# Kernel tuning notes

Hardware: AMD Instinct MI355X
Metric: run time of the kernel (lower is better)

The kernel has to match this reference:

```python
import jax, jax.numpy as jnp
import numpy as np

E = 8          # number of routed experts
TOP_K = 2      # experts per token
D = 2048       # hidden size
DFF = 1408     # per-expert intermediate
DFF_S = 2816   # shared-expert intermediate (2 shared experts fused)
B, S = 2, 2048


def setup_inputs() -> dict:
    key = jax.random.key(0)
    ks = jax.random.split(key, 8)
    sc = 0.02
    return {
        "hidden_states": jax.random.normal(ks[0], (B, S, D), jnp.float32),
        "gate_weight": jax.random.normal(ks[1], (E, D), jnp.float32) * sc,
        "w_gate": jax.random.normal(ks[2], (E, DFF, D), jnp.float32) * sc,
        "w_up": jax.random.normal(ks[3], (E, DFF, D), jnp.float32) * sc,
        "w_down": jax.random.normal(ks[4], (E, D, DFF), jnp.float32) * sc,
        "w_shared_gate": jax.random.normal(ks[5], (DFF_S, D), jnp.float32) * sc,
        "w_shared_up": jax.random.normal(ks[6], (DFF_S, D), jnp.float32) * sc,
        "w_shared_down": jax.random.normal(ks[7], (D, DFF_S), jnp.float32) * sc,
    }


def reference(hidden_states, gate_weight, w_gate, w_up, w_down,
              w_shared_gate, w_shared_up, w_shared_down):
    orig_shape = hidden_states.shape
    x = hidden_states.reshape(-1, orig_shape[-1])      # [T, D]

    # --- router (computed under no_grad in the original) ---
    logits = x @ gate_weight.T                          # [T, E]
    scores = jax.nn.softmax(logits, axis=-1)
    topk_w, topk_idx = jax.lax.top_k(scores, TOP_K)     # [T, K]
    topk_w = topk_w / jnp.sum(topk_w, axis=-1, keepdims=True)
    topk_w = jax.lax.stop_gradient(topk_w)
    topk_idx = jax.lax.stop_gradient(topk_idx)

    # dense combine weights [T, E] (equivalent to the masked per-expert loop +
    # weighted sum over the top-k copies)
    combine = jnp.einsum('tk,tke->te', topk_w,
                         jax.nn.one_hot(topk_idx, E, dtype=x.dtype))

    # --- routed experts: SwiGLU MLP per expert, dense over E ---
    g = jnp.einsum('td,efd->etf', x, w_gate)            # [E, T, DFF]
    u = jnp.einsum('td,efd->etf', x, w_up)
    h = jax.nn.silu(g) * u
    expert_out = jnp.einsum('etf,edf->etd', h, w_down)  # [E, T, D]
    y = jnp.einsum('etd,te->td', expert_out, combine)   # [T, D]

    # --- shared experts on the identity ---
    sh = jax.nn.silu(x @ w_shared_gate.T) * (x @ w_shared_up.T)
    y = y + sh @ w_shared_down.T

    return y.reshape(orig_shape)
```

## Files before the change

kernel.cpp:

```cpp
#include <hip/hip_runtime.h>
#include <stdint.h>
#include <stdio.h>

#define T_TOK 4096
#define DMODEL 2048
#define NEXP 8
#define DFF 1408
#define DFFS 2816
#define NSLOT 8192

#define GU_GRID (16 * 22 + 39 * 11)
#define DN_GRID (16 * 8 + 39 * 8)

typedef unsigned short u16;
typedef short s16x8 __attribute__((ext_vector_type(8)));
typedef unsigned short u16x4 __attribute__((ext_vector_type(4)));
typedef __bf16 bf16x8 __attribute__((ext_vector_type(8)));
typedef float f32x4 __attribute__((ext_vector_type(4)));

__device__ __forceinline__ u16 f2bf(float f) {
  uint32_t u = __builtin_bit_cast(uint32_t, f);
  u += 0x7fffu + ((u >> 16) & 1u);
  return (u16)(u >> 16);
}
__device__ __forceinline__ float bf2f(u16 h) {
  uint32_t u = ((uint32_t)h) << 16;
  return __builtin_bit_cast(float, u);
}

__device__ __forceinline__ void gl16(const u16* g, u16* l) {
  __builtin_amdgcn_global_load_lds((const __attribute__((address_space(1))) void*)g,
                                   (__attribute__((address_space(3))) void*)l,
                                   16, 0, 0);
}

#define BARRIER() asm volatile("s_barrier" ::: "memory")

__global__ void k_convert(const float* __restrict__ in, u16* __restrict__ out, int n8) {
  int i = blockIdx.x * 256 + threadIdx.x;
  if (i >= n8) return;
  float4 a = ((const float4*)in)[2 * i];
  float4 b = ((const float4*)in)[2 * i + 1];
  s16x8 r;
  r[0] = (short)f2bf(a.x); r[1] = (short)f2bf(a.y);
  r[2] = (short)f2bf(a.z); r[3] = (short)f2bf(a.w);
  r[4] = (short)f2bf(b.x); r[5] = (short)f2bf(b.y);
  r[6] = (short)f2bf(b.z); r[7] = (short)f2bf(b.w);
  ((s16x8*)out)[i] = r;
}

__global__ void k_zero(int* __restrict__ counts) {
  if (threadIdx.x < NEXP) counts[threadIdx.x] = 0;
}

__global__ void k_router(const float* __restrict__ x, const float* __restrict__ gw,
                         u16* __restrict__ xb,
                         float* __restrict__ tkw, int* __restrict__ tki,
                         int* __restrict__ counts) {
  __shared__ double sm[NEXP];
  int t = blockIdx.x;
  int tid = threadIdx.x;
  int lane = tid & 63, wv = tid >> 6;
  const float4* xr = (const float4*)(x + (size_t)t * DMODEL);
  const float4* gr = (const float4*)gw;
  int e0 = wv * 2, e1 = e0 + 1;
  double a0 = 0.0, a1 = 0.0;
#pragma unroll
  for (int it = 0; it < DMODEL / 4 / 64; ++it) {
    int idx = it * 64 + lane;
    float4 xv = xr[idx];
    float4 g0 = gr[e0 * (DMODEL / 4) + idx];
    float4 g1 = gr[e1 * (DMODEL / 4) + idx];
    a0 += (double)xv.x * g0.x + (double)xv.y * g0.y +
          (double)xv.z * g0.z + (double)xv.w * g0.w;
    a1 += (double)xv.x * g1.x + (double)xv.y * g1.y +
          (double)xv.z * g1.z + (double)xv.w * g1.w;
    if (wv == 0) {
      u16x4 r = { f2bf(xv.x), f2bf(xv.y), f2bf(xv.z), f2bf(xv.w) };
      ((u16x4*)(xb + (size_t)t * DMODEL))[idx] = r;
    }
  }
#pragma unroll
  for (int off = 32; off; off >>= 1) {
    a0 += __shfl_down(a0, off, 64);
    a1 += __shfl_down(a1, off, 64);
  }
  if (lane == 0) { sm[e0] = a0; sm[e1] = a1; }
  __syncthreads();
  if (tid == 0) {
    double acc[NEXP];
#pragma unroll
    for (int e = 0; e < NEXP; ++e) acc[e] = sm[e];
    int i0 = 0; double v0 = acc[0];
    for (int e = 1; e < NEXP; ++e) if (acc[e] > v0) { v0 = acc[e]; i0 = e; }
    int i1 = -1; double v1 = -1e300;
    for (int e = 0; e < NEXP; ++e) if (e != i0 && acc[e] > v1) { v1 = acc[e]; i1 = e; }
    double r = exp(v1 - v0);
    float w0 = (float)(1.0 / (1.0 + r));
    float w1 = 1.0f - w0;
    tkw[2 * t] = w0; tkw[2 * t + 1] = w1;
    tki[2 * t] = i0; tki[2 * t + 1] = i1;
    atomicAdd(&counts[i0], 1);
    atomicAdd(&counts[i1], 1);
  }
}

__global__ void k_scan(const int* __restrict__ counts, int* __restrict__ offs,
                       int* __restrict__ cursor) {
  if (threadIdx.x == 0) {
    int s = 0;
    for (int e = 0; e < NEXP; ++e) { offs[e] = s; cursor[e] = s; s += counts[e]; }
    offs[NEXP] = s;
  }
}

__global__ void k_assign(const int* __restrict__ tki, int* __restrict__ cursor,
                         int* __restrict__ pos, int* __restrict__ slot_tok) {
  int t = blockIdx.x * 256 + threadIdx.x;
  if (t >= T_TOK) return;
#pragma unroll
  for (int k = 0; k < 2; ++k) {
    int e = tki[2 * t + k];
    int p = atomicAdd(&cursor[e], 1);
    pos[2 * t + k] = p;
    slot_tok[p] = t;
  }
}

__global__ void k_sched(const int* __restrict__ counts, int* __restrict__ tblGU,
                        int* __restrict__ tblDN, int* __restrict__ nact) {
  if (threadIdx.x != 0 || blockIdx.x != 0) return;
  int g = 0, d = 0;
  for (int m = 0; m < T_TOK / 256; ++m) {
    for (int nb = 0; nb < DFFS * 2 / 256; ++nb)
      tblGU[g++] = (int)(0x80000000u | (m << 12) | nb);
    for (int nb = 0; nb < DMODEL / 256; ++nb)
      tblDN[d++] = (int)(0x80000000u | (m << 12) | nb);
  }
  for (int e = 0; e < NEXP; ++e) {
    int mb = (counts[e] + 255) >> 8;
    for (int m = 0; m < mb; ++m) {
      for (int nb = 0; nb < DFF * 2 / 256; ++nb)
        tblGU[g++] = (e << 24) | (m << 12) | nb;
      for (int nb = 0; nb < DMODEL / 256; ++nb)
        tblDN[d++] = (e << 24) | (m << 12) | nb;
    }
  }
  nact[0] = g; nact[1] = d;
}

template <int PHASE>
__launch_bounds__(512, 2)
__global__ void k_gemm8(const int* __restrict__ tbl, const int* __restrict__ nact,
                        const u16* __restrict__ xb,
                        const u16* __restrict__ hr, const u16* __restrict__ hs,
                        const u16* __restrict__ wbg, const u16* __restrict__ wbu,
                        const u16* __restrict__ wbd,
                        const u16* __restrict__ wbsg, const u16* __restrict__ wbsu,
                        const u16* __restrict__ wbsd,
                        u16* __restrict__ P1r, u16* __restrict__ P2r,
                        u16* __restrict__ P1s, u16* __restrict__ P2s,
                        u16* __restrict__ yr, float* __restrict__ out,
                        const int* __restrict__ offs, const int* __restrict__ counts,
                        const int* __restrict__ slot_tok) {
  __shared__ __attribute__((aligned(16))) u16 lds[2 * 32768];

  if ((int)blockIdx.x >= nact[PHASE]) return;
  const int desc = tbl[blockIdx.x];
  const bool shrd = desc < 0;
  const int e = (desc >> 24) & 0xF;
  const int m0 = ((desc >> 12) & 0xFFF) * 256;
  const int n0 = (desc & 0xFFF) * 256;

  const u16 *A, *B1, *B2;
  u16 *C1, *C2;
  float* OF = nullptr;
  int base, cnt, nsplit, K;
  bool gather = false;
  if constexpr (PHASE == 0) {
    K = DMODEL;
    if (shrd) {
      A = xb; base = 0; cnt = T_TOK;
      B1 = wbsg; B2 = wbsu; C1 = P1s; C2 = P2s; nsplit = DFFS;
    } else {
      A = xb; gather = true; base = offs[e]; cnt = counts[e];
      size_t es = (size_t)e * DFF * DMODEL;
      B1 = wbg + es; B2 = wbu + es; C1 = P1r; C2 = P2r; nsplit = DFF;
    }
  } else {
    nsplit = DMODEL;
    if (shrd) {
      A = hs; base = 0; cnt = T_TOK; K = DFFS;
      B1 = B2 = wbsd; OF = out; C1 = C2 = nullptr;
    } else {
      A = hr; base = offs[e]; cnt = counts[e]; K = DFF;
      B1 = B2 = wbd + (size_t)e * DMODEL * DFF; C1 = C2 = yr;
    }
  }
  const int NT = K >> 6;

  int tid = threadIdx.x;
  int lane = tid & 63, wv = tid >> 6;
  int wm = wv >> 2, wn = wv & 3;
  int fr = lane & 15, fq = lane >> 4;

  int srow = tid >> 3;
  int sslot = (tid & 7) ^ (srow & 7);
  const u16* ap[4]; const u16* bp[4];
#pragma unroll
  for (int h = 0; h < 4; ++h) {
    int r = h * 64 + srow;
    int ra = m0 + r; ra = ra < cnt ? ra : cnt - 1;
    int ga = gather ? slot_tok[base + ra] : base + ra;
    ap[h] = A + (size_t)ga * K + sslot * 8;
    int nc = n0 + r;
    const u16* bb = (nc >= nsplit) ? (B2 + (size_t)(nc - nsplit) * K)
                                   : (B1 + (size_t)nc * K);
    bp[h] = bb + sslot * 8;
  }

#define STG_A(h, bufi, kt) gl16(ap[h] + (size_t)(kt) * 64, \
                                lds + (bufi) * 32768 + (h) * 4096 + wv * 512)
#define STG_B(h, bufi, kt) gl16(bp[h] + (size_t)(kt) * 64, \
                                lds + (bufi) * 32768 + 16384 + (h) * 4096 + wv * 512)

  int sKs0 = ((0 + fq) ^ (fr & 7)) * 8;
  int sKs1 = ((4 + fq) ^ (fr & 7)) * 8;
  int aBase = wm * 8192 + fr * 64;
  int bBase = 16384 + (wn >> 1) * 8192 + ((wn & 1) * 64 + fr) * 64;

  f32x4 acc[8][4];
#pragma unroll
  for (int i = 0; i < 8; ++i)
#pragma unroll
    for (int j = 0; j < 4; ++j) acc[i][j] = (f32x4){0.f, 0.f, 0.f, 0.f};

  STG_A(0, 0, 0); STG_A(2, 0, 0);
  STG_B(0, 0, 0); STG_B(1, 0, 0);
  STG_B(2, 0, 0); STG_B(3, 0, 0);
  STG_A(1, 0, 0); STG_A(3, 0, 0);
  STG_A(0, 1, 1); STG_A(2, 1, 1);

  bf16x8 af[4][2], bkA[2][2], bkB[2][2];
  for (int t = 0; t < NT; ++t) {
    const int buf = t & 1, nbuf = buf ^ 1;
    const u16* lbuf = lds + buf * 32768;
    const bool hn1 = (t + 1) < NT, hn2 = (t + 2) < NT;

    if (t == NT - 1) asm volatile("s_waitcnt vmcnt(2)" ::: "memory");
    else             asm volatile("s_waitcnt vmcnt(4)" ::: "memory");
    BARRIER();
    __builtin_amdgcn_sched_barrier(0);
#pragma unroll
    for (int il = 0; il < 4; ++il) {
      af[il][0] = *(const bf16x8*)(lbuf + aBase + il * 1024 + sKs0);
      af[il][1] = *(const bf16x8*)(lbuf + aBase + il * 1024 + sKs1);
    }
#pragma unroll
    for (int jl = 0; jl < 2; ++jl) {
      bkA[jl][0] = *(const bf16x8*)(lbuf + bBase + jl * 1024 + sKs0);
      bkA[jl][1] = *(const bf16x8*)(lbuf + bBase + jl * 1024 + sKs1);
    }
    if (hn1) { STG_B(0, nbuf, t + 1); STG_B(1, nbuf, t + 1); }
    asm volatile("s_waitcnt lgkmcnt(0)" ::: "memory");
    __builtin_amdgcn_sched_barrier(0);
    __builtin_amdgcn_s_setprio(1);
#pragma unroll
    for (int il = 0; il < 4; ++il)
#pragma unroll
      for (int jl = 0; jl < 2; ++jl) {
        acc[il][jl] = __builtin_amdgcn_mfma_f32_16x16x32_bf16(af[il][0], bkA[jl][0], acc[il][jl], 0, 0, 0);
        acc[il][jl] = __builtin_amdgcn_mfma_f32_16x16x32_bf16(af[il][1], bkA[jl][1], acc[il][jl], 0, 0, 0);
      }
    __builtin_amdgcn_s_setprio(0);
    __builtin_amdgcn_sched_barrier(0);

    BARRIER();
    __builtin_amdgcn_sched_barrier(0);
#pragma unroll
    for (int jl = 0; jl < 2; ++jl) {
      bkB[jl][0] = *(const bf16x8*)(lbuf + bBase + (2 + jl) * 1024 + sKs0);
      bkB[jl][1] = *(const bf16x8*)(lbuf + bBase + (2 + jl) * 1024 + sKs1);
    }
    if (hn1) { STG_B(2, nbuf, t + 1); STG_B(3, nbuf, t + 1); }
    asm volatile("s_waitcnt lgkmcnt(0)" ::: "memory");
    __builtin_amdgcn_sched_barrier(0);
    __builtin_amdgcn_s_setprio(1);
#pragma unroll
    for (int il = 0; il < 4; ++il)
#pragma unroll
      for (int jl = 0; jl < 2; ++jl) {
        acc[il][2 + jl] = __builtin_amdgcn_mfma_f32_16x16x32_bf16(af[il][0], bkB[jl][0], acc[il][2 + jl], 0, 0, 0);
        acc[il][2 + jl] = __builtin_amdgcn_mfma_f32_16x16x32_bf16(af[il][1], bkB[jl][1], acc[il][2 + jl], 0, 0, 0);
      }
    __builtin_amdgcn_s_setprio(0);
    __builtin_amdgcn_sched_barrier(0);

    if (t == NT - 1) asm volatile("s_waitcnt vmcnt(0)" ::: "memory");
    else             asm volatile("s_waitcnt vmcnt(6)" ::: "memory");
    BARRIER();
    __builtin_amdgcn_sched_barrier(0);
#pragma unroll
    for (int il = 0; il < 4; ++il) {
      af[il][0] = *(const bf16x8*)(lbuf + aBase + (4 + il) * 1024 + sKs0);
      af[il][1] = *(const bf16x8*)(lbuf + aBase + (4 + il) * 1024 + sKs1);
    }
    if (hn1) { STG_A(1, nbuf, t + 1); STG_A(3, nbuf, t + 1); }
    asm volatile("s_waitcnt lgkmcnt(0)" ::: "memory");
    __builtin_amdgcn_sched_barrier(0);
    __builtin_amdgcn_s_setprio(1);
#pragma unroll
    for (int il = 0; il < 4; ++il)
#pragma unroll
      for (int jl = 0; jl < 2; ++jl) {
        acc[4 + il][jl] = __builtin_amdgcn_mfma_f32_16x16x32_bf16(af[il][0], bkA[jl][0], acc[4 + il][jl], 0, 0, 0);
        acc[4 + il][jl] = __builtin_amdgcn_mfma_f32_16x16x32_bf16(af[il][1], bkA[jl][1], acc[4 + il][jl], 0, 0, 0);
      }
    __builtin_amdgcn_s_setprio(0);
    __builtin_amdgcn_sched_barrier(0);

    BARRIER();
    __builtin_amdgcn_sched_barrier(0);
#pragma unroll
    for (int jl = 0; jl < 2; ++jl) {
      bkB[jl][0] = *(const bf16x8*)(lbuf + bBase + (2 + jl) * 1024 + sKs0);
      bkB[jl][1] = *(const bf16x8*)(lbuf + bBase + (2 + jl) * 1024 + sKs1);
    }
    if (hn2) { STG_A(0, buf, t + 2); STG_A(2, buf, t + 2); }
    asm volatile("s_waitcnt lgkmcnt(0)" ::: "memory");
    __builtin_amdgcn_sched_barrier(0);
    __builtin_amdgcn_s_setprio(1);
#pragma unroll
    for (int il = 0; il < 4; ++il)
#pragma unroll
      for (int jl = 0; jl < 2; ++jl) {
        acc[4 + il][2 + jl] = __builtin_amdgcn_mfma_f32_16x16x32_bf16(af[il][0], bkB[jl][0], acc[4 + il][2 + jl], 0, 0, 0);
        acc[4 + il][2 + jl] = __builtin_amdgcn_mfma_f32_16x16x32_bf16(af[il][1], bkB[jl][1], acc[4 + il][2 + jl], 0, 0, 0);
      }
    __builtin_amdgcn_s_setprio(0);
    __builtin_amdgcn_sched_barrier(0);
  }
#undef STG_A
#undef STG_B

#pragma unroll
  for (int i = 0; i < 8; ++i) {
    int row_t = wm * 128 + i * 16 + fq * 4;
#pragma unroll
    for (int r = 0; r < 4; ++r) {
      int m = m0 + row_t + r;
      if (m >= cnt) continue;
      size_t rowoff = (size_t)(base + m) * (size_t)nsplit;
#pragma unroll
      for (int j = 0; j < 4; ++j) {
        int col_t = n0 + wn * 64 + j * 16 + fr;
        float v = acc[i][j][r];
        if (PHASE == 1 && shrd)      OF[rowoff + col_t] = v;
        else if (col_t >= nsplit)    C2[rowoff + col_t - nsplit] = f2bf(v);
        else                         C1[rowoff + col_t] = f2bf(v);
      }
    }
  }
}

__global__ void k_silu2(const u16* __restrict__ g1, const u16* __restrict__ u1,
                        u16* __restrict__ h1, int n1,
                        const u16* __restrict__ g2, const u16* __restrict__ u2,
                        u16* __restrict__ h2, int n2) {
  int i = blockIdx.x * 256 + threadIdx.x;
  const u16 *g, *u; u16* h; int idx;
  if (i < n1) { g = g1; u = u1; h = h1; idx = i; }
  else { idx = i - n1; if (idx >= n2) return; g = g2; u = u2; h = h2; }
  s16x8 gv = ((const s16x8*)g)[idx];
  s16x8 uv = ((const s16x8*)u)[idx];
  s16x8 hv;
#pragma unroll
  for (int j = 0; j < 8; ++j) {
    float gf = bf2f((u16)gv[j]);
    float uf = bf2f((u16)uv[j]);
    float s = gf / (1.f + __expf(-gf));
    hv[j] = (short)f2bf(s * uf);
  }
  ((s16x8*)h)[idx] = hv;
}

__global__ void k_combine(float* __restrict__ y, const u16* __restrict__ yr,
                          const float* __restrict__ tkw, const int* __restrict__ pos) {
  int t = blockIdx.x;
  int i = threadIdx.x;
  float w0 = tkw[2 * t], w1 = tkw[2 * t + 1];
  size_t p0 = (size_t)pos[2 * t] * DMODEL, p1 = (size_t)pos[2 * t + 1] * DMODEL;
  int d0 = i * 8;
  s16x8 a = *(const s16x8*)(yr + p0 + d0);
  s16x8 b = *(const s16x8*)(yr + p1 + d0);
  float* yo = y + (size_t)t * DMODEL + d0;
#pragma unroll
  for (int j = 0; j < 8; ++j)
    yo[j] += w0 * bf2f((u16)a[j]) + w1 * bf2f((u16)b[j]);
}

extern "C" void kernel_launch(void* const* d_in, const int* in_sizes, int n_in,
                              void* d_out, int out_size, void* d_ws, size_t ws_size,
                              hipStream_t stream) {
  const float* x   = (const float*)d_in[0];
  const float* gw  = (const float*)d_in[1];
  const float* wg  = (const float*)d_in[2];
  const float* wu  = (const float*)d_in[3];
  const float* wd  = (const float*)d_in[4];
  const float* wsg = (const float*)d_in[5];
  const float* wsu = (const float*)d_in[6];
  const float* wsd = (const float*)d_in[7];
  float* out = (float*)d_out;

  char* ws = (char*)d_ws;
  size_t o = 0;
  auto alloc = [&](size_t bytes) -> void* {
    void* p = ws + o;
    o += (bytes + 255) & ~(size_t)255;
    return p;
  };
  u16* xb   = (u16*)alloc((size_t)T_TOK * DMODEL * 2);
  u16* wbg  = (u16*)alloc((size_t)NEXP * DFF * DMODEL * 2);
  u16* wbu  = (u16*)alloc((size_t)NEXP * DFF * DMODEL * 2);
  u16* wbd  = (u16*)alloc((size_t)NEXP * DMODEL * DFF * 2);
  u16* wbsg = (u16*)alloc((size_t)DFFS * DMODEL * 2);
  u16* wbsu = (u16*)alloc((size_t)DFFS * DMODEL * 2);
  u16* wbsd = (u16*)alloc((size_t)DMODEL * DFFS * 2);
  u16* P1r  = (u16*)alloc((size_t)NSLOT * DFF * 2);
  u16* P1s  = (u16*)alloc((size_t)T_TOK * DFFS * 2);
  u16* P2r  = (u16*)alloc((size_t)NSLOT * DFF * 2);
  u16* P2s  = (u16*)alloc((size_t)T_TOK * DFFS * 2);
  u16* yr   = P2r;
  float* tkw = (float*)alloc((size_t)T_TOK * 2 * 4);
  int* tki   = (int*)alloc((size_t)T_TOK * 2 * 4);
  int* pos   = (int*)alloc((size_t)T_TOK * 2 * 4);
  int* slot_tok = (int*)alloc((size_t)NSLOT * 4);
  int* counts   = (int*)alloc(64);
  int* offs     = (int*)alloc(64);
  int* cursor   = (int*)alloc(64);
  int* tblGU    = (int*)alloc(GU_GRID * 4);
  int* tblDN    = (int*)alloc(DN_GRID * 4);
  int* nact     = (int*)alloc(64);
  if (o > ws_size) {
    fprintf(stderr, "kernel_launch: ws too small: need %zu have %zu\n", o, ws_size);
    return;
  }

  {
    int n8w = NEXP * DFF * DMODEL / 8;
    k_convert<<<(n8w + 255) / 256, 256, 0, stream>>>(wg, wbg, n8w);
    k_convert<<<(n8w + 255) / 256, 256, 0, stream>>>(wu, wbu, n8w);
    k_convert<<<(n8w + 255) / 256, 256, 0, stream>>>(wd, wbd, n8w);
    int n8s = DFFS * DMODEL / 8;
    k_convert<<<(n8s + 255) / 256, 256, 0, stream>>>(wsg, wbsg, n8s);
    k_convert<<<(n8s + 255) / 256, 256, 0, stream>>>(wsu, wbsu, n8s);
    k_convert<<<(n8s + 255) / 256, 256, 0, stream>>>(wsd, wbsd, n8s);
  }

  k_zero<<<1, 64, 0, stream>>>(counts);
  k_router<<<T_TOK, 256, 0, stream>>>(x, gw, xb, tkw, tki, counts);
  k_scan<<<1, 64, 0, stream>>>(counts, offs, cursor);
  k_assign<<<(T_TOK + 255) / 256, 256, 0, stream>>>(tki, cursor, pos, slot_tok);
  k_sched<<<1, 64, 0, stream>>>(counts, tblGU, tblDN, nact);

  k_gemm8<0><<<GU_GRID, 512, 0, stream>>>(
      tblGU, nact, xb, nullptr, nullptr,
      wbg, wbu, wbd, wbsg, wbsu, wbsd,
      P1r, P2r, P1s, P2s, yr, out, offs, counts, slot_tok);

  {
    int n1 = NSLOT * DFF / 8, n2 = T_TOK * DFFS / 8;
    k_silu2<<<(n1 + n2 + 255) / 256, 256, 0, stream>>>(
        P1r, P2r, P1r, n1, P1s, P2s, P1s, n2);
  }

  k_gemm8<1><<<DN_GRID, 512, 0, stream>>>(
      tblDN, nact, xb, P1r, P1s,
      wbg, wbu, wbd, wbsg, wbsu, wbsd,
      P1r, P2r, P1s, P2s, yr, out, offs, counts, slot_tok);

  k_combine<<<T_TOK, 256, 0, stream>>>(out, yr, tkw, pos);
}
```

Baseline: 590.4 us.

## Fuse weight conversions, merge scan/sched kernels, and software-pipeline GEMM LDS reads

Merges the six fp32-to-bf16 weight conversion launches into one grid-stride kernel and folds the scan and schedule-table kernels into a single launch. It also restructures the GEMM main loop so the next tile's A/B fragments are read from LDS while the current MFMAs run, cutting the barriers per K-step from four to two. This is meant to reduce launch overhead and LDS-read stalls in the GEMMs. In exchange it needs more fragment registers, which may hurt occupancy, and it changes the vmcnt wait accounting, which must stay correct.

```diff
diff --git a/kernel.cpp b/kernel.cpp
--- a/kernel.cpp
+++ b/kernel.cpp
@@ -36,17 +36,39 @@
 
 #define BARRIER() asm volatile("s_barrier" ::: "memory")
 
-__global__ void k_convert(const float* __restrict__ in, u16* __restrict__ out, int n8) {
-  int i = blockIdx.x * 256 + threadIdx.x;
-  if (i >= n8) return;
-  float4 a = ((const float4*)in)[2 * i];
-  float4 b = ((const float4*)in)[2 * i + 1];
-  s16x8 r;
-  r[0] = (short)f2bf(a.x); r[1] = (short)f2bf(a.y);
-  r[2] = (short)f2bf(a.z); r[3] = (short)f2bf(a.w);
-  r[4] = (short)f2bf(b.x); r[5] = (short)f2bf(b.y);
-  r[6] = (short)f2bf(b.z); r[7] = (short)f2bf(b.w);
-  ((s16x8*)out)[i] = r;
+__global__ void k_convert6(const float* __restrict__ s0, u16* __restrict__ d0, int n0,
+                           const float* __restrict__ s1, u16* __restrict__ d1, int n1,
+                           const float* __restrict__ s2, u16* __restrict__ d2, int n2,
+                           const float* __restrict__ s3, u16* __restrict__ d3, int n3,
+                           const float* __restrict__ s4, u16* __restrict__ d4, int n4,
+                           const float* __restrict__ s5, u16* __restrict__ d5, int n5) {
+  int total = n0 + n1 + n2 + n3 + n4 + n5;
+  int stride = gridDim.x * 256;
+  for (int i = blockIdx.x * 256 + threadIdx.x; i < total; i += stride) {
+    const float* s; u16* d; int k = i;
+    if (k < n0) { s = s0; d = d0; }
+    else { k -= n0;
+      if (k < n1) { s = s1; d = d1; }
+      else { k -= n1;
+        if (k < n2) { s = s2; d = d2; }
+        else { k -= n2;
+          if (k < n3) { s = s3; d = d3; }
+          else { k -= n3;
+            if (k < n4) { s = s4; d = d4; }
+            else { k -= n4; s = s5; d = d5; }
+          }
+        }
+      }
+    }
+    float4 a = ((const float4*)s)[2 * k];
+    float4 b = ((const float4*)s)[2 * k + 1];
+    s16x8 r;
+    r[0] = (short)f2bf(a.x); r[1] = (short)f2bf(a.y);
+    r[2] = (short)f2bf(a.z); r[3] = (short)f2bf(a.w);
+    r[4] = (short)f2bf(b.x); r[5] = (short)f2bf(b.y);
+    r[6] = (short)f2bf(b.z); r[7] = (short)f2bf(b.w);
+    ((s16x8*)d)[k] = r;
+  }
 }
 
 __global__ void k_zero(int* __restrict__ counts) {
@@ -105,31 +127,13 @@
   }
 }
 
-__global__ void k_scan(const int* __restrict__ counts, int* __restrict__ offs,
-                       int* __restrict__ cursor) {
-  if (threadIdx.x == 0) {
-    int s = 0;
-    for (int e = 0; e < NEXP; ++e) { offs[e] = s; cursor[e] = s; s += counts[e]; }
-    offs[NEXP] = s;
-  }
-}
-
-__global__ void k_assign(const int* __restrict__ tki, int* __restrict__ cursor,
-                         int* __restrict__ pos, int* __restrict__ slot_tok) {
-  int t = blockIdx.x * 256 + threadIdx.x;
-  if (t >= T_TOK) return;
-#pragma unroll
-  for (int k = 0; k < 2; ++k) {
-    int e = tki[2 * t + k];
-    int p = atomicAdd(&cursor[e], 1);
-    pos[2 * t + k] = p;
-    slot_tok[p] = t;
-  }
-}
-
-__global__ void k_sched(const int* __restrict__ counts, int* __restrict__ tblGU,
-                        int* __restrict__ tblDN, int* __restrict__ nact) {
+__global__ void k_scan_sched(const int* __restrict__ counts, int* __restrict__ offs,
+                             int* __restrict__ cursor, int* __restrict__ tblGU,
+                             int* __restrict__ tblDN, int* __restrict__ nact) {
   if (threadIdx.x != 0 || blockIdx.x != 0) return;
+  int s = 0;
+  for (int e = 0; e < NEXP; ++e) { offs[e] = s; cursor[e] = s; s += counts[e]; }
+  offs[NEXP] = s;
   int g = 0, d = 0;
   for (int m = 0; m < T_TOK / 256; ++m) {
     for (int nb = 0; nb < DFFS * 2 / 256; ++nb)
@@ -147,6 +151,19 @@
     }
   }
   nact[0] = g; nact[1] = d;
+}
+
+__global__ void k_assign(const int* __restrict__ tki, int* __restrict__ cursor,
+                         int* __restrict__ pos, int* __restrict__ slot_tok) {
+  int t = blockIdx.x * 256 + threadIdx.x;
+  if (t >= T_TOK) return;
+#pragma unroll
+  for (int k = 0; k < 2; ++k) {
+    int e = tki[2 * t + k];
+    int p = atomicAdd(&cursor[e], 1);
+    pos[2 * t + k] = p;
+    slot_tok[p] = t;
+  }
 }
 
 template <int PHASE>
@@ -235,110 +252,104 @@
 #pragma unroll
     for (int j = 0; j < 4; ++j) acc[i][j] = (f32x4){0.f, 0.f, 0.f, 0.f};
 
-  STG_A(0, 0, 0); STG_A(2, 0, 0);
-  STG_B(0, 0, 0); STG_B(1, 0, 0);
-  STG_B(2, 0, 0); STG_B(3, 0, 0);
-  STG_A(1, 0, 0); STG_A(3, 0, 0);
-  STG_A(0, 1, 1); STG_A(2, 1, 1);
-
-  bf16x8 af[4][2], bkA[2][2], bkB[2][2];
+  STG_A(0, 0, 0); STG_A(1, 0, 0); STG_A(2, 0, 0); STG_A(3, 0, 0);
+  STG_B(0, 0, 0); STG_B(1, 0, 0); STG_B(2, 0, 0); STG_B(3, 0, 0);
+  if (NT > 1) { STG_A(0, 1, 1); STG_A(1, 1, 1); STG_A(2, 1, 1); STG_A(3, 1, 1); }
+  if (NT > 1) asm volatile("s_waitcnt vmcnt(4)" ::: "memory");
+  else        asm volatile("s_waitcnt vmcnt(0)" ::: "memory");
+  BARRIER();
+  __builtin_amdgcn_sched_barrier(0);
+
+  bf16x8 rAa[4][2], rAb[4][2], rB01[2][2], rB23[2][2];
+#pragma unroll
+  for (int il = 0; il < 4; ++il) {
+    rAa[il][0] = *(const bf16x8*)(lds + aBase + il * 1024 + sKs0);
+    rAa[il][1] = *(const bf16x8*)(lds + aBase + il * 1024 + sKs1);
+  }
+#pragma unroll
+  for (int jl = 0; jl < 2; ++jl) {
+    rB01[jl][0] = *(const bf16x8*)(lds + bBase + jl * 1024 + sKs0);
+    rB01[jl][1] = *(const bf16x8*)(lds + bBase + jl * 1024 + sKs1);
+  }
+
   for (int t = 0; t < NT; ++t) {
     const int buf = t & 1, nbuf = buf ^ 1;
     const u16* lbuf = lds + buf * 32768;
+    const u16* lbufN = lds + nbuf * 32768;
     const bool hn1 = (t + 1) < NT, hn2 = (t + 2) < NT;
 
-    if (t == NT - 1) asm volatile("s_waitcnt vmcnt(2)" ::: "memory");
-    else             asm volatile("s_waitcnt vmcnt(4)" ::: "memory");
+#pragma unroll
+    for (int jl = 0; jl < 2; ++jl) {
+      rB23[jl][0] = *(const bf16x8*)(lbuf + bBase + (2 + jl) * 1024 + sKs0);
+      rB23[jl][1] = *(const bf16x8*)(lbuf + bBase + (2 + jl) * 1024 + sKs1);
+    }
+    if (hn1) { STG_B(0, nbuf, t + 1); STG_B(1, nbuf, t + 1); }
+    __builtin_amdgcn_s_setprio(1);
+#pragma unroll
+    for (int il = 0; il < 4; ++il)
+#pragma unroll
+      for (int jl = 0; jl < 2; ++jl) {
+        acc[il][jl] = __builtin_amdgcn_mfma_f32_16x16x32_bf16(rAa[il][0], rB01[jl][0], acc[il][jl], 0, 0, 0);
+        acc[il][jl] = __builtin_amdgcn_mfma_f32_16x16x32_bf16(rAa[il][1], rB01[jl][1], acc[il][jl], 0, 0, 0);
+      }
+    __builtin_amdgcn_s_setprio(0);
+
+#pragma unroll
+    for (int il = 0; il < 4; ++il) {
+      rAb[il][0] = *(const bf16x8*)(lbuf + aBase + (4 + il) * 1024 + sKs0);
+      rAb[il][1] = *(const bf16x8*)(lbuf + aBase + (4 + il) * 1024 + sKs1);
+    }
+    if (hn1) { STG_B(2, nbuf, t + 1); STG_B(3, nbuf, t + 1); }
+    __builtin_amdgcn_s_setprio(1);
+#pragma unroll
+    for (int il = 0; il < 4; ++il)
+#pragma unroll
+      for (int jl = 0; jl < 2; ++jl) {
+        acc[il][2 + jl] = __builtin_amdgcn_mfma_f32_16x16x32_bf16(rAa[il][0], rB23[jl][0], acc[il][2 + jl], 0, 0, 0);
+        acc[il][2 + jl] = __builtin_amdgcn_mfma_f32_16x16x32_bf16(rAa[il][1], rB23[jl][1], acc[il][2 + jl], 0, 0, 0);
+      }
+    __builtin_amdgcn_s_setprio(0);
+
+    asm volatile("s_waitcnt lgkmcnt(0)" ::: "memory");
     BARRIER();
     __builtin_amdgcn_sched_barrier(0);
-#pragma unroll
-    for (int il = 0; il < 4; ++il) {
-      af[il][0] = *(const bf16x8*)(lbuf + aBase + il * 1024 + sKs0);
-      af[il][1] = *(const bf16x8*)(lbuf + aBase + il * 1024 + sKs1);
-    }
-#pragma unroll
-    for (int jl = 0; jl < 2; ++jl) {
-      bkA[jl][0] = *(const bf16x8*)(lbuf + bBase + jl * 1024 + sKs0);
-      bkA[jl][1] = *(const bf16x8*)(lbuf + bBase + jl * 1024 + sKs1);
-    }
-    if (hn1) { STG_B(0, nbuf, t + 1); STG_B(1, nbuf, t + 1); }
-    asm volatile("s_waitcnt lgkmcnt(0)" ::: "memory");
-    __builtin_amdgcn_sched_barrier(0);
+    if (hn2) { STG_A(0, buf, t + 2); STG_A(1, buf, t + 2); }
     __builtin_amdgcn_s_setprio(1);
 #pragma unroll
     for (int il = 0; il < 4; ++il)
 #pragma unroll
       for (int jl = 0; jl < 2; ++jl) {
-        acc[il][jl] = __builtin_amdgcn_mfma_f32_16x16x32_bf16(af[il][0], bkA[jl][0], acc[il][jl], 0, 0, 0);
-        acc[il][jl] = __builtin_amdgcn_mfma_f32_16x16x32_bf16(af[il][1], bkA[jl][1], acc[il][jl], 0, 0, 0);
+        acc[4 + il][jl] = __builtin_amdgcn_mfma_f32_16x16x32_bf16(rAb[il][0], rB01[jl][0], acc[4 + il][jl], 0, 0, 0);
+        acc[4 + il][jl] = __builtin_amdgcn_mfma_f32_16x16x32_bf16(rAb[il][1], rB01[jl][1], acc[4 + il][jl], 0, 0, 0);
       }
     __builtin_amdgcn_s_setprio(0);
-    __builtin_amdgcn_sched_barrier(0);
-
-    BARRIER();
-    __builtin_amdgcn_sched_barrier(0);
-#pragma unroll
-    for (int jl = 0; jl < 2; ++jl) {
-      bkB[jl][0] = *(const bf16x8*)(lbuf + bBase + (2 + jl) * 1024 + sKs0);
-      bkB[jl][1] = *(const bf16x8*)(lbuf + bBase + (2 + jl) * 1024 + sKs1);
-    }
-    if (hn1) { STG_B(2, nbuf, t + 1); STG_B(3, nbuf, t + 1); }
-    asm volatile("s_waitcnt lgkmcnt(0)" ::: "memory");
-    __builtin_amdgcn_sched_barrier(0);
+
+    if (hn1) {
+      if (hn2) asm volatile("s_waitcnt vmcnt(2)" ::: "memory");
+      else     asm volatile("s_waitcnt vmcnt(0)" ::: "memory");
+      BARRIER();
+      __builtin_amdgcn_sched_barrier(0);
+      if (hn2) { STG_A(2, buf, t + 2); STG_A(3, buf, t + 2); }
+#pragma unroll
+      for (int il = 0; il < 4; ++il) {
+        rAa[il][0] = *(const bf16x8*)(lbufN + aBase + il * 1024 + sKs0);
+        rAa[il][1] = *(const bf16x8*)(lbufN + aBase + il * 1024 + sKs1);
+      }
+#pragma unroll
+      for (int jl = 0; jl < 2; ++jl) {
+        rB01[jl][0] = *(const bf16x8*)(lbufN + bBase + jl * 1024 + sKs0);
+        rB01[jl][1] = *(const bf16x8*)(lbufN + bBase + jl * 1024 + sKs1);
+      }
+    }
     __builtin_amdgcn_s_setprio(1);
 #pragma unroll
     for (int il = 0; il < 4; ++il)
 #pragma unroll
       for (int jl = 0; jl < 2; ++jl) {
-        acc[il][2 + jl] = __builtin_amdgcn_mfma_f32_16x16x32_bf16(af[il][0], bkB[jl][0], acc[il][2 + jl], 0, 0, 0);
-        acc[il][2 + jl] = __builtin_amdgcn_mfma_f32_16x16x32_bf16(af[il][1], bkB[jl][1], acc[il][2 + jl], 0, 0, 0);
+        acc[4 + il][2 + jl] = __builtin_amdgcn_mfma_f32_16x16x32_bf16(rAb[il][0], rB23[jl][0], acc[4 + il][2 + jl], 0, 0, 0);
+        acc[4 + il][2 + jl] = __builtin_amdgcn_mfma_f32_16x16x32_bf16(rAb[il][1], rB23[jl][1], acc[4 + il][2 + jl], 0, 0, 0);
       }
     __builtin_amdgcn_s_setprio(0);
-    __builtin_amdgcn_sched_barrier(0);
-
-    if (t == NT - 1) asm volatile("s_waitcnt vmcnt(0)" ::: "memory");
-    else             asm volatile("s_waitcnt vmcnt(6)" ::: "memory");
-    BARRIER();
-    __builtin_amdgcn_sched_barrier(0);
-#pragma unroll
-    for (int il = 0; il < 4; ++il) {
-      af[il][0] = *(const bf16x8*)(lbuf + aBase + (4 + il) * 1024 + sKs0);
-      af[il][1] = *(const bf16x8*)(lbuf + aBase + (4 + il) * 1024 + sKs1);
-    }
-    if (hn1) { STG_A(1, nbuf, t + 1); STG_A(3, nbuf, t + 1); }
-    asm volatile("s_waitcnt lgkmcnt(0)" ::: "memory");
-    __builtin_amdgcn_sched_barrier(0);
-    __builtin_amdgcn_s_setprio(1);
-#pragma unroll
-    for (int il = 0; il < 4; ++il)
-#pragma unroll
-      for (int jl = 0; jl < 2; ++jl) {
-        acc[4 + il][jl] = __builtin_amdgcn_mfma_f32_16x16x32_bf16(af[il][0], bkA[jl][0], acc[4 + il][jl], 0, 0, 0);
-        acc[4 + il][jl] = __builtin_amdgcn_mfma_f32_16x16x32_bf16(af[il][1], bkA[jl][1], acc[4 + il][jl], 0, 0, 0);
-      }
-    __builtin_amdgcn_s_setprio(0);
-    __builtin_amdgcn_sched_barrier(0);
-
-    BARRIER();
-    __builtin_amdgcn_sched_barrier(0);
-#pragma unroll
-    for (int jl = 0; jl < 2; ++jl) {
-      bkB[jl][0] = *(const bf16x8*)(lbuf + bBase + (2 + jl) * 1024 + sKs0);
-      bkB[jl][1] = *(const bf16x8*)(lbuf + bBase + (2 + jl) * 1024 + sKs1);
-    }
-    if (hn2) { STG_A(0, buf, t + 2); STG_A(2, buf, t + 2); }
-    asm volatile("s_waitcnt lgkmcnt(0)" ::: "memory");
-    __builtin_amdgcn_sched_barrier(0);
-    __builtin_amdgcn_s_setprio(1);
-#pragma unroll
-    for (int il = 0; il < 4; ++il)
-#pragma unroll
-      for (int jl = 0; jl < 2; ++jl) {
-        acc[4 + il][2 + jl] = __builtin_amdgcn_mfma_f32_16x16x32_bf16(af[il][0], bkB[jl][0], acc[4 + il][2 + jl], 0, 0, 0);
-        acc[4 + il][2 + jl] = __builtin_amdgcn_mfma_f32_16x16x32_bf16(af[il][1], bkB[jl][1], acc[4 + il][2 + jl], 0, 0, 0);
-      }
-    __builtin_amdgcn_s_setprio(0);
-    __builtin_amdgcn_sched_barrier(0);
   }
 #undef STG_A
 #undef STG_B
@@ -448,20 +459,15 @@
 
   {
     int n8w = NEXP * DFF * DMODEL / 8;
-    k_convert<<<(n8w + 255) / 256, 256, 0, stream>>>(wg, wbg, n8w);
-    k_convert<<<(n8w + 255) / 256, 256, 0, stream>>>(wu, wbu, n8w);
-    k_convert<<<(n8w + 255) / 256, 256, 0, stream>>>(wd, wbd, n8w);
     int n8s = DFFS * DMODEL / 8;
-    k_convert<<<(n8s + 255) / 256, 256, 0, stream>>>(wsg, wbsg, n8s);
-    k_convert<<<(n8s + 255) / 256, 256, 0, stream>>>(wsu, wbsu, n8s);
-    k_convert<<<(n8s + 255) / 256, 256, 0, stream>>>(wsd, wbsd, n8s);
+    k_convert6<<<2048, 256, 0, stream>>>(wg, wbg, n8w, wu, wbu, n8w, wd, wbd, n8w,
+                                         wsg, wbsg, n8s, wsu, wbsu, n8s, wsd, wbsd, n8s);
   }
 
   k_zero<<<1, 64, 0, stream>>>(counts);
   k_router<<<T_TOK, 256, 0, stream>>>(x, gw, xb, tkw, tki, counts);
-  k_scan<<<1, 64, 0, stream>>>(counts, offs, cursor);
+  k_scan_sched<<<1, 64, 0, stream>>>(counts, offs, cursor, tblGU, tblDN, nact);
   k_assign<<<(T_TOK + 255) / 256, 256, 0, stream>>>(tki, cursor, pos, slot_tok);
-  k_sched<<<1, 64, 0, stream>>>(counts, tblGU, tblDN, nact);
 
   k_gemm8<0><<<GU_GRID, 512, 0, stream>>>(
       tblGU, nact, xb, nullptr, nullptr,
```

Measured after the change: 584.7 us. Within noise of the previous version (-1.0%).
